# Kernel optimization log

Measured on AMD Instinct MI355X. Metric: run time of the kernel, lower is better.

The kernel has to match this reference:

```python
import jax, jax.numpy as jnp
import numpy as np

N_AUTHOR = 100000
N_PAPER = 200000
D = 128          # embedding_dim
E = 600000       # edges (used in both directions: author->paper and paper->author)
S = 100000       # supervision edges
L = 2            # n_layers


def setup_inputs() -> dict:
    key = jax.random.key(0)
    ks = jax.random.split(key, 14)
    s = 1.0 / np.sqrt(D)
    return {
        "x_author": jax.random.normal(ks[0], (N_AUTHOR, D), jnp.float32),
        "x_paper": jax.random.normal(ks[1], (N_PAPER, D), jnp.float32),
        "edge_author": jax.random.randint(ks[2], (E,), 0, N_AUTHOR, jnp.int32),
        "edge_paper": jax.random.randint(ks[3], (E,), 0, N_PAPER, jnp.int32),
        "sup_author": jax.random.randint(ks[4], (S,), 0, N_AUTHOR, jnp.int32),
        "sup_paper": jax.random.randint(ks[5], (S,), 0, N_PAPER, jnp.int32),
        # per-layer stacked Linear params (W is [in, out]; equivalent to torch x @ W.T + b)
        "W_self_author": jax.random.uniform(ks[6], (L, D, D), jnp.float32, -s, s),
        "b_self_author": jax.random.uniform(ks[7], (L, D), jnp.float32, -s, s),
        "W_self_paper": jax.random.uniform(ks[8], (L, D, D), jnp.float32, -s, s),
        "b_self_paper": jax.random.uniform(ks[9], (L, D), jnp.float32, -s, s),
        "W_a2p": jax.random.uniform(ks[10], (L, D, D), jnp.float32, -s, s),  # message_('author','writes','paper')
        "b_a2p": jax.random.uniform(ks[11], (L, D), jnp.float32, -s, s),
        "W_p2a": jax.random.uniform(ks[12], (L, D, D), jnp.float32, -s, s),  # message_('paper','rev_writes','author')
        "b_p2a": jax.random.uniform(ks[13], (L, D), jnp.float32, -s, s),
    }


def reference(x_author, x_paper, edge_author, edge_paper, sup_author, sup_paper,
              W_self_author, b_self_author, W_self_paper, b_self_paper,
              W_a2p, b_a2p, W_p2a, b_p2a):
    n_layers = W_self_author.shape[0]
    n_author = x_author.shape[0]
    n_paper = x_paper.shape[0]
    for l in range(n_layers):
        # gather src features -> per-edge linear -> scatter-sum to dst (aggr='sum')
        msg_to_paper = jax.ops.segment_sum(
            x_author[edge_author] @ W_a2p[l] + b_a2p[l], edge_paper, num_segments=n_paper)
        msg_to_author = jax.ops.segment_sum(
            x_paper[edge_paper] @ W_p2a[l] + b_p2a[l], edge_author, num_segments=n_author)
        # self-loop projection + aggregated incoming messages
        new_author = x_author @ W_self_author[l] + b_self_author[l] + msg_to_author
        new_paper = x_paper @ W_self_paper[l] + b_self_paper[l] + msg_to_paper
        if l < n_layers - 1:  # nonlinearity between layers
            new_author = jax.nn.relu(new_author)
            new_paper = jax.nn.relu(new_paper)
        x_author, x_paper = new_author, new_paper
    # supervision link scores: dot product of paired embeddings
    return (x_author[sup_author] * x_paper[sup_paper]).sum(axis=-1)
```

## Files before the change

### kernel.cpp

```cpp
#include <hip/hip_runtime.h>
#include <stdint.h>

#define D 128
#define SCAN_TILE 1024
#define CB_SHIFT 11
#define CB_NODES 2048
#define CHE 2048

typedef __attribute__((ext_vector_type(8))) short bf16x8_t;
typedef __attribute__((ext_vector_type(4))) float f32x4_t;

__device__ inline unsigned short f2bf(float x) {
    unsigned int u = __float_as_uint(x);
    unsigned int r = (u + 0x7fffu + ((u >> 16) & 1u)) >> 16;
    return (unsigned short)r;
}
__device__ inline float bflo(unsigned v) { return __uint_as_float(v << 16); }
__device__ inline float bfhi(unsigned v) { return __uint_as_float(v & 0xffff0000u); }

__global__ __launch_bounds__(256) void f32_to_bf16_duo(
        const float* __restrict__ inA, unsigned short* __restrict__ outA, int n8A,
        const float* __restrict__ inP, unsigned short* __restrict__ outP, int n8P) {
    int stride = gridDim.x * blockDim.x;
    int total = n8A + n8P;
    for (int i = blockIdx.x * blockDim.x + threadIdx.x; i < total; i += stride) {
        const float* in; unsigned short* out; int j;
        if (i < n8A) { in = inA; out = outA; j = i; }
        else         { in = inP; out = outP; j = i - n8A; }
        float4 v0 = *(const float4*)(in + (size_t)j * 8);
        float4 v1 = *(const float4*)(in + (size_t)j * 8 + 4);
        uint4 o;
        o.x = f2bf(v0.x) | ((unsigned)f2bf(v0.y) << 16);
        o.y = f2bf(v0.z) | ((unsigned)f2bf(v0.w) << 16);
        o.z = f2bf(v1.x) | ((unsigned)f2bf(v1.y) << 16);
        o.w = f2bf(v1.z) | ((unsigned)f2bf(v1.w) << 16);
        *(uint4*)(out + (size_t)j * 8) = o;
    }
}

__global__ void count_deg_kernel(const int* __restrict__ ea, const int* __restrict__ ep,
                                 int E, int* __restrict__ degA, int* __restrict__ degP) {
    int stride = gridDim.x * blockDim.x;
    for (int e = blockIdx.x * blockDim.x + threadIdx.x; e < E; e += stride) {
        atomicAdd(&degA[ea[e]], 1);
        atomicAdd(&degP[ep[e]], 1);
    }
}

__global__ __launch_bounds__(256) void scan_partials_kernel(
        const int* __restrict__ degA, int nA,
        const int* __restrict__ degP, int nP, int gA,
        int* __restrict__ partials) {
    const int* deg; int n;
    int b = blockIdx.x;
    if (b < gA) { deg = degA; n = nA; }
    else        { deg = degP; n = nP; b -= gA; }
    int tid = threadIdx.x;
    int i0 = b * SCAN_TILE + tid * 4;
    int s = 0;
    if (i0 + 3 < n) {
        int4 d = *(const int4*)(deg + i0);
        s = d.x + d.y + d.z + d.w;
    } else {
        for (int j = 0; j < 4; ++j) if (i0 + j < n) s += deg[i0 + j];
    }
#pragma unroll
    for (int off = 32; off; off >>= 1) s += __shfl_xor(s, off);
    __shared__ int wsum[4];
    if ((tid & 63) == 0) wsum[tid >> 6] = s;
    __syncthreads();
    if (tid == 0) partials[blockIdx.x] = wsum[0] + wsum[1] + wsum[2] + wsum[3];
}

__global__ __launch_bounds__(1024) void scan_block_sums_kernel(
        int* __restrict__ partials, int gA, int gP,
        int* __restrict__ rsA_end, int* __restrict__ rsP_end) {
    __shared__ int s[1024];
    int n = gA + gP;
    int tid = threadIdx.x;
    int v = (tid < n) ? partials[tid] : 0;
    s[tid] = v;
    __syncthreads();
    for (int off = 1; off < 1024; off <<= 1) {
        int add = 0;
        if (tid >= off && ((tid < gA) || (tid - off >= gA))) add = s[tid - off];
        __syncthreads();
        s[tid] += add;
        __syncthreads();
    }
    if (tid == gA - 1)  *rsA_end = s[tid];
    if (tid == n - 1)   *rsP_end = s[tid];
    if (tid < n) partials[tid] = s[tid] - v;
}

__global__ __launch_bounds__(256) void scan_write_kernel(
        const int* __restrict__ degA, int nA, int* __restrict__ rsA,
        const int* __restrict__ degP, int nP, int* __restrict__ rsP,
        int gA, const int* __restrict__ partials) {
    const int* deg; int n; int* rs;
    int b = blockIdx.x;
    int part = partials[blockIdx.x];
    if (b < gA) { deg = degA; n = nA; rs = rsA; }
    else        { deg = degP; n = nP; rs = rsP; b -= gA; }
    int tid = threadIdx.x;
    int lane = tid & 63, wid = tid >> 6;
    int i0 = b * SCAN_TILE + tid * 4;

    int4 d = make_int4(0, 0, 0, 0);
    if (i0 + 3 < n) {
        d = *(const int4*)(deg + i0);
    } else {
        if (i0 + 0 < n) d.x = deg[i0 + 0];
        if (i0 + 1 < n) d.y = deg[i0 + 1];
        if (i0 + 2 < n) d.z = deg[i0 + 2];
        if (i0 + 3 < n) d.w = deg[i0 + 3];
    }
    int tsum = d.x + d.y + d.z + d.w;

    int x = tsum;
#pragma unroll
    for (int off = 1; off < 64; off <<= 1) {
        int y = __shfl_up(x, off);
        if (lane >= off) x += y;
    }
    int excl = x - tsum;

    __shared__ int wsum[4];
    if (lane == 63) wsum[wid] = x;
    __syncthreads();
    int woff = 0;
#pragma unroll
    for (int w = 0; w < 4; ++w) if (w < wid) woff += wsum[w];

    int off0 = part + woff + excl;
    int4 o;
    o.x = off0;
    o.y = off0 + d.x;
    o.z = o.y + d.y;
    o.w = o.z + d.z;
    if (i0 + 3 < n) {
        *(int4*)(rs + i0) = o;
    } else {
        if (i0 + 0 < n) rs[i0 + 0] = o.x;
        if (i0 + 1 < n) rs[i0 + 1] = o.y;
        if (i0 + 2 < n) rs[i0 + 2] = o.z;
        if (i0 + 3 < n) rs[i0 + 3] = o.w;
    }
}

__global__ __launch_bounds__(256) void gcur_init_kernel(
        const int* __restrict__ rsA, int nbcA,
        const int* __restrict__ rsP, int nbc, int E, int* __restrict__ gcur) {
    int i = blockIdx.x * blockDim.x + threadIdx.x;
    if (i < nbcA)                gcur[i] = rsA[i << CB_SHIFT];
    else if (i < nbc)            gcur[i] = E + rsP[(i - nbcA) << CB_SHIFT];
}

__global__ __launch_bounds__(256) void multisplit_kernel(
        const int* __restrict__ ea, const int* __restrict__ ep, int E,
        int nbcA, int* __restrict__ gcur, unsigned* __restrict__ buf) {
    __shared__ int hist[256];
    __shared__ int off[256];
    __shared__ int cnt2[256];
    __shared__ int gbase[256];
    __shared__ unsigned cbuf[2 * CHE];
    __shared__ unsigned char bkt[2 * CHE];

    int tid = threadIdx.x;
    int e0 = blockIdx.x * CHE;
    int ecnt = E - e0; if (ecnt > CHE) ecnt = CHE;

    hist[tid] = 0;
    __syncthreads();

    for (int k = tid; k < ecnt; k += 256) {
        int a = ea[e0 + k], p = ep[e0 + k];
        atomicAdd(&hist[a >> CB_SHIFT], 1);
        atomicAdd(&hist[nbcA + (p >> CB_SHIFT)], 1);
    }
    __syncthreads();

    int v = hist[tid];
    off[tid] = v;
    __syncthreads();
    for (int o = 1; o < 256; o <<= 1) {
        int y = (tid >= o) ? off[tid - o] : 0;
        __syncthreads();
        off[tid] += y;
        __syncthreads();
    }
    int excl = off[tid] - v;
    off[tid] = excl;
    cnt2[tid] = 0;
    if (v > 0) gbase[tid] = atomicAdd(&gcur[tid], v);
    __syncthreads();

    for (int k = tid; k < ecnt; k += 256) {
        int a = ea[e0 + k], p = ep[e0 + k];
        int bA = a >> CB_SHIFT;
        int iA = off[bA] + atomicAdd(&cnt2[bA], 1);
        cbuf[iA] = ((unsigned)p << CB_SHIFT) | (unsigned)(a & (CB_NODES - 1));
        bkt[iA] = (unsigned char)bA;
        int bP = nbcA + (p >> CB_SHIFT);
        int iP = off[bP] + atomicAdd(&cnt2[bP], 1);
        cbuf[iP] = ((unsigned)a << CB_SHIFT) | (unsigned)(p & (CB_NODES - 1));
        bkt[iP] = (unsigned char)bP;
    }
    __syncthreads();

    int total = 2 * ecnt;
    for (int i = tid; i < total; i += 256) {
        int b = bkt[i];
        buf[(size_t)gbase[b] + (i - off[b])] = cbuf[i];
    }
}

__global__ __launch_bounds__(1024) void fine_csr_kernel(
        const int* __restrict__ rsA, int nA, int nbcA, int* __restrict__ csrA,
        const int* __restrict__ rsP, int nP, int* __restrict__ csrP,
        const unsigned* __restrict__ buf, int E) {
    __shared__ int base[CB_NODES + 1];
    __shared__ int cnt[CB_NODES];
    const int* rs; int* csr; int n; int d0; const unsigned* mybuf;
    int b = blockIdx.x;
    if (b < nbcA) { rs = rsA; csr = csrA; n = nA; d0 = b << CB_SHIFT; mybuf = buf; }
    else { rs = rsP; csr = csrP; n = nP; d0 = (b - nbcA) << CB_SHIFT; mybuf = buf + E; }
    int nd = n - d0; if (nd > CB_NODES) nd = CB_NODES;

    int tid = threadIdx.x;
    for (int i = tid; i <= nd; i += 1024) base[i] = rs[d0 + i];
    for (int i = tid; i < nd; i += 1024) cnt[i] = 0;
    __syncthreads();

    int g0 = base[0], g1 = base[nd];
    for (int j = g0 + tid; j < g1; j += 1024) {
        unsigned pk = mybuf[j];
        int li = pk & (CB_NODES - 1);
        int src = (int)(pk >> CB_SHIFT);
        int pos = base[li] + atomicAdd(&cnt[li], 1);
        csr[pos] = src;
    }
}

__global__ __launch_bounds__(256) void pack_w_kernel(
        const float* __restrict__ WsA, const float* __restrict__ WsP,
        const float* __restrict__ Wa2p, const float* __restrict__ Wp2a,
        unsigned short* __restrict__ Bpack) {
    int combo = blockIdx.x >> 4;
    int e = (blockIdx.x & 15) * 256 + threadIdx.x;
    int layer = combo >> 1;
    const float* Ws = ((combo & 1) ? WsP : WsA) + (size_t)layer * D * D;
    const float* Wm = ((combo & 1) ? Wa2p : Wp2a) + (size_t)layer * D * D;

    int f = e >> 6, lane = e & 63;
    int nf = f >> 3, ks = f & 7;
    int k0 = ks * 32 + (lane >> 4) * 8;
    int col = nf * 16 + (lane & 15);

    unsigned short v[8];
#pragma unroll
    for (int j = 0; j < 8; ++j) {
        int k = k0 + j;
        float x = (k < D) ? Ws[(size_t)k * D + col] : Wm[(size_t)(k - D) * D + col];
        v[j] = f2bf(x);
    }
    uint4 o;
    o.x = v[0] | ((unsigned)v[1] << 16);
    o.y = v[2] | ((unsigned)v[3] << 16);
    o.z = v[4] | ((unsigned)v[5] << 16);
    o.w = v[6] | ((unsigned)v[7] << 16);
    *(uint4*)(Bpack + (size_t)combo * 32768 + (size_t)e * 8) = o;
}

__global__ __launch_bounds__(256) void aggregate_duo(
        const unsigned short* __restrict__ srcA, const int* __restrict__ rsA,
        const int* __restrict__ csrA, int nA, unsigned short* __restrict__ aggA,
        const unsigned short* __restrict__ srcP, const int* __restrict__ rsP,
        const int* __restrict__ csrP, int nP, unsigned short* __restrict__ aggP) {
    int gw   = (blockIdx.x * 256 + threadIdx.x) >> 6;
    int lane = threadIdx.x & 63;
    int sub  = lane >> 4;
    int sl   = lane & 15;

    const unsigned short* xsrc; const int* rs; const int* csr;
    unsigned short* agg; int d;
    if (gw < nA) { d = gw;      xsrc = srcA; rs = rsA; csr = csrA; agg = aggA; }
    else {
        d = gw - nA;
        if (d >= nP) return;
        xsrc = srcP; rs = rsP; csr = csrP; agg = aggP;
    }

    int s0 = rs[d], s1 = rs[d + 1];
    float acc[8] = {0.f, 0.f, 0.f, 0.f, 0.f, 0.f, 0.f, 0.f};
    for (int j = s0 + sub; j < s1; j += 4) {
        int s = csr[j];
        uint4 v = *(const uint4*)(xsrc + (size_t)s * D + sl * 8);
        acc[0] += bflo(v.x); acc[1] += bfhi(v.x);
        acc[2] += bflo(v.y); acc[3] += bfhi(v.y);
        acc[4] += bflo(v.z); acc[5] += bfhi(v.z);
        acc[6] += bflo(v.w); acc[7] += bfhi(v.w);
    }
#pragma unroll
    for (int i = 0; i < 8; ++i) {
        acc[i] += __shfl_xor(acc[i], 16);
        acc[i] += __shfl_xor(acc[i], 32);
    }
    if (sub == 0) {
        uint4 o;
        o.x = f2bf(acc[0]) | ((unsigned)f2bf(acc[1]) << 16);
        o.y = f2bf(acc[2]) | ((unsigned)f2bf(acc[3]) << 16);
        o.z = f2bf(acc[4]) | ((unsigned)f2bf(acc[5]) << 16);
        o.w = f2bf(acc[6]) | ((unsigned)f2bf(acc[7]) << 16);
        *(uint4*)(agg + (size_t)d * D + sl * 8) = o;
    }
}

__global__ __launch_bounds__(256) void linear_mfma_duo(
        const unsigned short* __restrict__ xsA, const unsigned short* __restrict__ xmA,
        const unsigned short* __restrict__ BpA, const float* __restrict__ bsA,
        const float* __restrict__ bmA, const int* __restrict__ degA_, int nA,
        unsigned short* __restrict__ outA, int gmA,
        const unsigned short* __restrict__ xsP, const unsigned short* __restrict__ xmP,
        const unsigned short* __restrict__ BpP, const float* __restrict__ bsP,
        const float* __restrict__ bmP, const int* __restrict__ degP_, int nP,
        unsigned short* __restrict__ outP, int relu) {
    __shared__ uint4 lds4[2048];
    unsigned char* lds = (unsigned char*)lds4;
    int tid = threadIdx.x;
    int wave = tid >> 6, lane = tid & 63;

    const unsigned short *xs, *xm, *Bpack; const float *bs, *bm;
    const int* deg; int n; unsigned short* out;
    int b = blockIdx.x;
    if (b < gmA) { xs = xsA; xm = xmA; Bpack = BpA; bs = bsA; bm = bmA;
                   deg = degA_; n = nA; out = outA; }
    else { b -= gmA; xs = xsP; xm = xmP; Bpack = BpP; bs = bsP; bm = bmP;
           deg = degP_; n = nP; out = outP; }
    int r_base = b * 64;

#pragma unroll
    for (int i = 0; i < 8; ++i) {
        int c = i * 256 + tid;
        int row = c >> 5;
        int kc = (c & 31) * 8;
        int rg = r_base + row;
        uint4 w = make_uint4(0, 0, 0, 0);
        if (rg < n) {
            const unsigned short* src = (kc < D) ? (xs + (size_t)rg * D + kc)
                                                 : (xm + (size_t)rg * D + (kc - D));
            w = *(const uint4*)src;
        }
        unsigned addr = ((unsigned)(row * 512 + kc * 2)) ^ ((unsigned)((row & 7) << 4));
        *(uint4*)(lds + addr) = w;
    }
    __syncthreads();

    int lrow = wave * 16 + (lane & 15);
    bf16x8_t a[8];
#pragma unroll
    for (int ks = 0; ks < 8; ++ks) {
        unsigned addr = ((unsigned)(lrow * 512 + ks * 64 + (lane >> 4) * 16))
                        ^ ((unsigned)((lrow & 7) << 4));
        a[ks] = *(const bf16x8_t*)(lds + addr);
    }

    f32x4_t acc[8];
#pragma unroll
    for (int nf = 0; nf < 8; ++nf) acc[nf] = (f32x4_t){0.f, 0.f, 0.f, 0.f};

    const bf16x8_t* bp = (const bf16x8_t*)Bpack;
    bf16x8_t bcur[8], bnxt[8];
#pragma unroll
    for (int ks = 0; ks < 8; ++ks) bcur[ks] = bp[ks * 64 + lane];

#pragma unroll
    for (int nf = 0; nf < 8; ++nf) {
        if (nf < 7) {
#pragma unroll
            for (int ks = 0; ks < 8; ++ks)
                bnxt[ks] = bp[((nf + 1) * 8 + ks) * 64 + lane];
        }
#pragma unroll
        for (int ks = 0; ks < 8; ++ks)
            acc[nf] = __builtin_amdgcn_mfma_f32_16x16x32_bf16(a[ks], bcur[ks], acc[nf], 0, 0, 0);
#pragma unroll
        for (int ks = 0; ks < 8; ++ks) bcur[ks] = bnxt[ks];
    }

    int rb2 = r_base + wave * 16 + (lane >> 4) * 4;
    float dg[4];
#pragma unroll
    for (int rr = 0; rr < 4; ++rr)
        dg[rr] = (rb2 + rr < n) ? (float)deg[rb2 + rr] : 0.f;

#pragma unroll
    for (int nf = 0; nf < 8; ++nf) {
        int col = nf * 16 + (lane & 15);
        float bsv = bs[col], bmv = bm[col];
#pragma unroll
        for (int rr = 0; rr < 4; ++rr) {
            int r = rb2 + rr;
            if (r < n) {
                float v = acc[nf][rr] + bsv + dg[rr] * bmv;
                if (relu) v = fmaxf(v, 0.f);
                out[(size_t)r * D + col] = f2bf(v);
            }
        }
    }
}

__global__ __launch_bounds__(256) void dot_kernel(
        const unsigned short* __restrict__ za, const unsigned short* __restrict__ zp,
        const int* __restrict__ sa, const int* __restrict__ sp, int S,
        float* __restrict__ out) {
    int gw   = (blockIdx.x * 256 + threadIdx.x) >> 6;
    int lane = threadIdx.x & 63;
    int nw   = (gridDim.x * 256) >> 6;
    for (int i = gw; i < S; i += nw) {
        int a = sa[i], p = sp[i];
        unsigned ua = *(const unsigned*)(za + (size_t)a * D + lane * 2);
        unsigned up = *(const unsigned*)(zp + (size_t)p * D + lane * 2);
        float s = bflo(ua) * bflo(up) + bfhi(ua) * bfhi(up);
#pragma unroll
        for (int off = 32; off > 0; off >>= 1) s += __shfl_xor(s, off);
        if (lane == 0) out[i] = s;
    }
}

extern "C" void kernel_launch(void* const* d_in, const int* in_sizes, int n_in,
                              void* d_out, int out_size, void* d_ws, size_t ws_size,
                              hipStream_t stream) {
    const float* x_a  = (const float*)d_in[0];
    const float* x_p  = (const float*)d_in[1];
    const int*   ea   = (const int*)d_in[2];
    const int*   ep   = (const int*)d_in[3];
    const int*   sa   = (const int*)d_in[4];
    const int*   sp   = (const int*)d_in[5];
    const float* WsA  = (const float*)d_in[6];
    const float* bsA  = (const float*)d_in[7];
    const float* WsP  = (const float*)d_in[8];
    const float* bsP  = (const float*)d_in[9];
    const float* Wa2p = (const float*)d_in[10];
    const float* ba2p = (const float*)d_in[11];
    const float* Wp2a = (const float*)d_in[12];
    const float* bp2a = (const float*)d_in[13];

    const int nA = in_sizes[0] / D;
    const int nP = in_sizes[1] / D;
    const int E  = in_sizes[2];
    const int S  = in_sizes[4];

    char* ws = (char*)d_ws;
    size_t curoff = 0;
    auto alloc = [&](size_t bytes) -> void* {
        void* p = ws + curoff;
        curoff = (curoff + bytes + 255) & ~(size_t)255;
        return p;
    };
    unsigned short* xb_a  = (unsigned short*)alloc((size_t)nA * D * 2);
    unsigned short* xb_p  = (unsigned short*)alloc((size_t)nP * D * 2);
    unsigned short* agg_a = (unsigned short*)alloc((size_t)nA * D * 2);
    unsigned short* agg_p = (unsigned short*)alloc((size_t)nP * D * 2);
    unsigned short* y_a   = (unsigned short*)alloc((size_t)nA * D * 2);
    unsigned short* y_p   = (unsigned short*)alloc((size_t)nP * D * 2);
    unsigned short* z_a   = (unsigned short*)alloc((size_t)nA * D * 2);
    unsigned short* z_p   = (unsigned short*)alloc((size_t)nP * D * 2);
    int* degA = (int*)alloc((size_t)nA * 4);
    int* degP = (int*)alloc((size_t)nP * 4);
    int* rsA  = (int*)alloc(((size_t)nA + 1) * 4);
    int* rsP  = (int*)alloc(((size_t)nP + 1) * 4);
    int* csrA = (int*)alloc((size_t)E * 4);
    int* csrP = (int*)alloc((size_t)E * 4);
    const int gA = (nA + SCAN_TILE - 1) / SCAN_TILE;
    const int gP = (nP + SCAN_TILE - 1) / SCAN_TILE;
    int* partials = (int*)alloc((size_t)(gA + gP) * 4);
    unsigned short* Bpack = (unsigned short*)alloc((size_t)4 * 32768 * 2);

    const int nbcA = (nA + CB_NODES - 1) >> CB_SHIFT;
    const int nbcP = (nP + CB_NODES - 1) >> CB_SHIFT;
    const int NBC  = nbcA + nbcP;
    unsigned* buf = (unsigned*)z_a;
    int* gcur = (int*)z_p;

    f32_to_bf16_duo<<<3072, 256, 0, stream>>>(x_a, xb_a, nA * D / 8,
                                              x_p, xb_p, nP * D / 8);
    size_t deg_bytes = (size_t)((char*)degP - (char*)degA) + (size_t)nP * 4;
    hipMemsetAsync(degA, 0, deg_bytes, stream);
    pack_w_kernel<<<64, 256, 0, stream>>>(WsA, WsP, Wa2p, Wp2a, Bpack);
    count_deg_kernel<<<1024, 256, 0, stream>>>(ea, ep, E, degA, degP);
    scan_partials_kernel<<<gA + gP, 256, 0, stream>>>(degA, nA, degP, nP, gA, partials);
    scan_block_sums_kernel<<<1, 1024, 0, stream>>>(partials, gA, gP, rsA + nA, rsP + nP);
    scan_write_kernel<<<gA + gP, 256, 0, stream>>>(degA, nA, rsA,
                                                   degP, nP, rsP, gA, partials);
    gcur_init_kernel<<<1, 256, 0, stream>>>(rsA, nbcA, rsP, NBC, E, gcur);
    multisplit_kernel<<<(E + CHE - 1) / CHE, 256, 0, stream>>>(ea, ep, E, nbcA, gcur, buf);
    fine_csr_kernel<<<NBC, 1024, 0, stream>>>(rsA, nA, nbcA, csrA,
                                              rsP, nP, csrP, buf, E);

    const int gmA = (nA + 63) / 64;
    const int gmP = (nP + 63) / 64;
    const int gAgg = (nA + nP + 3) / 4;

    aggregate_duo<<<gAgg, 256, 0, stream>>>(xb_p, rsA, csrA, nA, agg_a,
                                            xb_a, rsP, csrP, nP, agg_p);
    linear_mfma_duo<<<gmA + gmP, 256, 0, stream>>>(
        xb_a, agg_a, Bpack + 0 * 32768, bsA, bp2a, degA, nA, y_a, gmA,
        xb_p, agg_p, Bpack + 1 * 32768, bsP, ba2p, degP, nP, y_p, 1);

    aggregate_duo<<<gAgg, 256, 0, stream>>>(y_p, rsA, csrA, nA, agg_a,
                                            y_a, rsP, csrP, nP, agg_p);
    linear_mfma_duo<<<gmA + gmP, 256, 0, stream>>>(
        y_a, agg_a, Bpack + 2 * 32768, bsA + D, bp2a + D, degA, nA, z_a, gmA,
        y_p, agg_p, Bpack + 3 * 32768, bsP + D, ba2p + D, degP, nP, z_p, 0);

    dot_kernel<<<(S + 3) / 4, 256, 0, stream>>>(z_a, z_p, sa, sp, S, (float*)d_out);
}
```

Baseline: 517.6 us.

## Split GEMM output columns across waves, keep weight slice in registers

Each wave of the node-update GEMM now owns a 32-column slice of the output for all 64 rows, instead of a 16-row slice across all 128 columns. Each wave loads only its quarter of the packed weight matrix into registers, issuing those loads before the LDS staging so they overlap the feature loads. Previously every wave streamed the whole weight matrix. The cost is four times as many LDS reads of the A tile per wave, and the degree lookup is now done per element rather than hoisted.

Result: faster. 478.9 us (-7.5%).

```diff
diff --git a/kernel.cpp b/kernel.cpp
--- a/kernel.cpp
+++ b/kernel.cpp
@@ -339,6 +339,14 @@
            deg = degP_; n = nP; out = outP; }
     int r_base = b * 64;
 
+    const bf16x8_t* bp = (const bf16x8_t*)Bpack;
+    bf16x8_t bb[2][8];
+#pragma unroll
+    for (int nf2 = 0; nf2 < 2; ++nf2)
+#pragma unroll
+        for (int ks = 0; ks < 8; ++ks)
+            bb[nf2][ks] = bp[((wave * 2 + nf2) * 8 + ks) * 64 + lane];
+
 #pragma unroll
     for (int i = 0; i < 8; ++i) {
         int c = i * 256 + tid;
@@ -356,55 +364,45 @@
     }
     __syncthreads();
 
-    int lrow = wave * 16 + (lane & 15);
-    bf16x8_t a[8];
-#pragma unroll
-    for (int ks = 0; ks < 8; ++ks) {
-        unsigned addr = ((unsigned)(lrow * 512 + ks * 64 + (lane >> 4) * 16))
-                        ^ ((unsigned)((lrow & 7) << 4));
-        a[ks] = *(const bf16x8_t*)(lds + addr);
-    }
-
-    f32x4_t acc[8];
-#pragma unroll
-    for (int nf = 0; nf < 8; ++nf) acc[nf] = (f32x4_t){0.f, 0.f, 0.f, 0.f};
-
-    const bf16x8_t* bp = (const bf16x8_t*)Bpack;
-    bf16x8_t bcur[8], bnxt[8];
-#pragma unroll
-    for (int ks = 0; ks < 8; ++ks) bcur[ks] = bp[ks * 64 + lane];
-
-#pragma unroll
-    for (int nf = 0; nf < 8; ++nf) {
-        if (nf < 7) {
-#pragma unroll
-            for (int ks = 0; ks < 8; ++ks)
-                bnxt[ks] = bp[((nf + 1) * 8 + ks) * 64 + lane];
+    f32x4_t acc[4][2];
+#pragma unroll
+    for (int rt = 0; rt < 4; ++rt)
+#pragma unroll
+        for (int nf2 = 0; nf2 < 2; ++nf2) acc[rt][nf2] = (f32x4_t){0.f, 0.f, 0.f, 0.f};
+
+#pragma unroll
+    for (int rt = 0; rt < 4; ++rt) {
+        int lrow = rt * 16 + (lane & 15);
+        bf16x8_t a[8];
+#pragma unroll
+        for (int ks = 0; ks < 8; ++ks) {
+            unsigned addr = ((unsigned)(lrow * 512 + ks * 64 + (lane >> 4) * 16))
+                            ^ ((unsigned)((lrow & 7) << 4));
+            a[ks] = *(const bf16x8_t*)(lds + addr);
         }
 #pragma unroll
-        for (int ks = 0; ks < 8; ++ks)
-            acc[nf] = __builtin_amdgcn_mfma_f32_16x16x32_bf16(a[ks], bcur[ks], acc[nf], 0, 0, 0);
-#pragma unroll
-        for (int ks = 0; ks < 8; ++ks) bcur[ks] = bnxt[ks];
-    }
-
-    int rb2 = r_base + wave * 16 + (lane >> 4) * 4;
-    float dg[4];
-#pragma unroll
-    for (int rr = 0; rr < 4; ++rr)
-        dg[rr] = (rb2 + rr < n) ? (float)deg[rb2 + rr] : 0.f;
-
-#pragma unroll
-    for (int nf = 0; nf < 8; ++nf) {
-        int col = nf * 16 + (lane & 15);
+        for (int ks = 0; ks < 8; ++ks) {
+            acc[rt][0] = __builtin_amdgcn_mfma_f32_16x16x32_bf16(a[ks], bb[0][ks], acc[rt][0], 0, 0, 0);
+            acc[rt][1] = __builtin_amdgcn_mfma_f32_16x16x32_bf16(a[ks], bb[1][ks], acc[rt][1], 0, 0, 0);
+        }
+    }
+
+#pragma unroll
+    for (int nf2 = 0; nf2 < 2; ++nf2) {
+        int col = wave * 32 + nf2 * 16 + (lane & 15);
         float bsv = bs[col], bmv = bm[col];
 #pragma unroll
-        for (int rr = 0; rr < 4; ++rr) {
-            int r = rb2 + rr;
-            if (r < n) {
-                float v = acc[nf][rr] + bsv + dg[rr] * bmv;
-                if (relu) v = fmaxf(v, 0.f);
-                out[(size_t)r * D + col] = f2bf(v);
+        for (int rt = 0; rt < 4; ++rt) {
+            int rb2 = r_base + rt * 16 + (lane >> 4) * 4;
+#pragma unroll
+            for (int rr = 0; rr < 4; ++rr) {
+                int r = rb2 + rr;
+                if (r < n) {
+                    float dgv = (float)deg[r];
+                    float v = acc[rt][nf2][rr] + bsv + dgv * bmv;
+                    if (relu) v = fmaxf(v, 0.f);
+                    out[(size_t)r * D + col] = f2bf(v);
+                }
             }
         }
     }
```
